# Performance work log

Measured on AMD Instinct MI355X. Metric: run time of the kernel, lower is better.

Reference implementation:

```python
import jax, jax.numpy as jnp
import numpy as np

B, S, H, L, NH, DH, FF = 64, 128, 768, 6, 12, 64, 3072
VOCAB, MAXPOS, INTENT, TAGS = 30522, 512, 22, 122
LN_EPS = 1e-12
INV_SQRT_DH = float(1.0 / np.sqrt(DH))


def _ln(x, s, b):
    m = x.mean(-1, keepdims=True)
    v = ((x - m) ** 2).mean(-1, keepdims=True)
    return (x - m) * jax.lax.rsqrt(v + LN_EPS) * s + b


def setup_inputs():
    key = jax.random.key(0)
    cnt = [0]
    def nk():
        cnt[0] += 1
        return jax.random.fold_in(key, cnt[0])
    def nrm(shape):
        return (0.02 * jax.random.normal(nk(), shape)).astype(jnp.float32)
    inp = {
        'input_ids': jax.random.randint(nk(), (B, S), 0, VOCAB),
        'attention_mask': jnp.ones((B, S), jnp.int32),
        'intent_target': jax.random.randint(nk(), (B,), 0, INTENT),
        'slots_target': jax.random.randint(nk(), (B, S), 0, TAGS),
        'slots_mask': jnp.ones((B, S), jnp.int32),
        'word_emb': nrm((VOCAB, H)), 'pos_emb': nrm((MAXPOS, H)),
        'emb_ln_s': jnp.ones((H,)), 'emb_ln_b': jnp.zeros((H,)),
        'Wq': nrm((L, H, H)), 'bq': jnp.zeros((L, H)),
        'Wk': nrm((L, H, H)), 'bk': jnp.zeros((L, H)),
        'Wv': nrm((L, H, H)), 'bv': jnp.zeros((L, H)),
        'Wo': nrm((L, H, H)), 'bo': jnp.zeros((L, H)),
        'sa_ln_s': jnp.ones((L, H)), 'sa_ln_b': jnp.zeros((L, H)),
        'W1f': nrm((L, H, FF)), 'b1f': jnp.zeros((L, FF)),
        'W2f': nrm((L, FF, H)), 'b2f': jnp.zeros((L, H)),
        'out_ln_s': jnp.ones((L, H)), 'out_ln_b': jnp.zeros((L, H)),
        'iW1': nrm((H, 64)), 'ib1': jnp.zeros((64,)),
        'iW2': nrm((64, INTENT)), 'ib2': jnp.zeros((INTENT,)),
        'sW1': nrm((H, 256)), 'sb1': jnp.zeros((256,)),
        'sW2': nrm((256, TAGS)), 'sb2': jnp.zeros((TAGS,)),
        'crf_start': nrm((TAGS,)), 'crf_end': nrm((TAGS,)), 'crf_trans': nrm((TAGS, TAGS)),
        'log_vars': jnp.zeros((2,)),
    }
    return inp


def _encoder(input_ids, attention_mask, word_emb, pos_emb, emb_ln_s, emb_ln_b,
             Wq, bq, Wk, bk, Wv, bv, Wo, bo, sa_ln_s, sa_ln_b,
             W1f, b1f, W2f, b2f, out_ln_s, out_ln_b):
    x = word_emb[input_ids] + pos_emb[jnp.arange(S)][None]
    x = _ln(x, emb_ln_s, emb_ln_b)
    neg = jnp.where(attention_mask[:, None, None, :] > 0, 0.0, -1e9).astype(x.dtype)
    for i in range(L):
        q = (x @ Wq[i] + bq[i]).reshape(B, S, NH, DH).transpose(0, 2, 1, 3)
        k = (x @ Wk[i] + bk[i]).reshape(B, S, NH, DH).transpose(0, 2, 1, 3)
        v = (x @ Wv[i] + bv[i]).reshape(B, S, NH, DH).transpose(0, 2, 1, 3)
        scores = jnp.einsum('bhqd,bhkd->bhqk', q, k) * INV_SQRT_DH + neg
        attn = jax.nn.softmax(scores, -1)
        ctx = jnp.einsum('bhqk,bhkd->bhqd', attn, v).transpose(0, 2, 1, 3).reshape(B, S, H)
        x = _ln(x + ctx @ Wo[i] + bo[i], sa_ln_s[i], sa_ln_b[i])
        h = jax.nn.gelu(x @ W1f[i] + b1f[i], approximate=False) @ W2f[i] + b2f[i]
        x = _ln(x + h, out_ln_s[i], out_ln_b[i])
    return x


def _crf_llh(emis, tags, mask, crf_start, crf_end, crf_trans):
    # pytorch-crf log-likelihood, reduction='sum'. emis [B,S,T], mask bool [B,S]
    fmask = mask.astype(emis.dtype)
    emit_sc = jnp.take_along_axis(emis, tags[..., None], -1)[..., 0]          # [B,S]
    trans_sc = crf_trans[tags[:, :-1], tags[:, 1:]]                            # [B,S-1]
    last_idx = mask.sum(1) - 1
    last_tag = tags[jnp.arange(B), last_idx]
    num = (crf_start[tags[:, 0]] + emit_sc[:, 0]
           + ((trans_sc + emit_sc[:, 1:]) * fmask[:, 1:]).sum(1)
           + crf_end[last_tag])
    def fstep(alpha, xs):
        emit_t, m_t = xs
        nxt = jax.nn.logsumexp(alpha[:, :, None] + crf_trans[None] + emit_t[:, None, :], axis=1)
        return jnp.where(m_t[:, None], nxt, alpha), None
    alpha0 = crf_start[None] + emis[:, 0]
    alpha, _ = jax.lax.scan(fstep, alpha0, (emis[:, 1:].transpose(1, 0, 2), mask[:, 1:].T))
    denom = jax.nn.logsumexp(alpha + crf_end[None], -1)
    return jnp.sum(num - denom)


def _viterbi(emis, mask, crf_start, crf_end, crf_trans):
    ident = jnp.arange(TAGS)[None, :]
    def vstep(alpha, xs):
        emit_t, m_t = xs
        score = alpha[:, :, None] + crf_trans[None] + emit_t[:, None, :]      # [B,T,T]
        bp = jnp.where(m_t[:, None], jnp.argmax(score, 1), ident)
        alpha = jnp.where(m_t[:, None], jnp.max(score, 1), alpha)
        return alpha, bp
    alpha0 = crf_start[None] + emis[:, 0]
    alpha, bps = jax.lax.scan(vstep, alpha0, (emis[:, 1:].transpose(1, 0, 2), mask[:, 1:].T))
    last = jnp.argmax(alpha + crf_end[None], -1)                               # [B]
    def bstep(tag, bp):
        prev = jnp.take_along_axis(bp, tag[:, None], 1)[:, 0]
        return prev, prev
    _, prevs = jax.lax.scan(bstep, last, bps, reverse=True)                    # [S-1,B]
    return jnp.concatenate([prevs, last[None]], 0).T                           # [B,S]


def reference(input_ids, attention_mask, intent_target, slots_target, slots_mask,
              word_emb, pos_emb, emb_ln_s, emb_ln_b,
              Wq, bq, Wk, bk, Wv, bv, Wo, bo, sa_ln_s, sa_ln_b,
              W1f, b1f, W2f, b2f, out_ln_s, out_ln_b,
              iW1, ib1, iW2, ib2, sW1, sb1, sW2, sb2,
              crf_start, crf_end, crf_trans, log_vars):
    x = _encoder(input_ids, attention_mask, word_emb, pos_emb, emb_ln_s, emb_ln_b,
                 Wq, bq, Wk, bk, Wv, bv, Wo, bo, sa_ln_s, sa_ln_b,
                 W1f, b1f, W2f, b2f, out_ln_s, out_ln_b)
    # intent head: linear1(relu(cls)) -> relu -> linear2 (dropout = eval identity)
    intent_logits = jax.nn.relu(jax.nn.relu(x[:, 0]) @ iW1 + ib1) @ iW2 + ib2
    intent_loss = (jax.nn.logsumexp(intent_logits, -1)
                   - jnp.take_along_axis(intent_logits, intent_target[:, None], 1)[:, 0])
    intent_pred = jnp.argmax(intent_logits, -1)
    # slots head
    slots_logits = jax.nn.relu(jax.nn.relu(x) @ sW1 + sb1) @ sW2 + sb2
    mask = slots_mask.astype(bool)
    slots_loss = -_crf_llh(slots_logits, slots_target, mask, crf_start, crf_end, crf_trans)
    p1 = jnp.exp(-log_vars[0])
    p2 = jnp.exp(-log_vars[1])
    joint_loss = jnp.sum(p1 * intent_loss + log_vars[0]) + (p2 * slots_loss + log_vars[1])
    slots_pred = _viterbi(slots_logits, mask, crf_start, crf_end, crf_trans)
    return joint_loss, slots_pred, intent_pred
```

## Files before the change

### kernel.cpp

```cpp
#include <hip/hip_runtime.h>
#include <math.h>
#include <stdint.h>

#define B_      64
#define S_      128
#define H_      768
#define L_      6
#define NH_     12
#define DH_     64
#define FF_     3072
#define INTENT_ 22
#define TAGS_   122
#define NT_     (B_*S_)
#define LN_EPS  1e-12f
#define INV_SQRT_DH 0.125f

#define GF_RELU_OUT 2
#define GF_GELU_OUT 4
#define GF_ADDRES   16
#define GF_ACCH     32

typedef _Float16 half8 __attribute__((ext_vector_type(8)));
typedef float    f32x4 __attribute__((ext_vector_type(4)));

__device__ __forceinline__ void gld16(const _Float16* g, _Float16* l) {
    __builtin_amdgcn_global_load_lds(
        (const __attribute__((address_space(1))) unsigned int*)(uintptr_t)g,
        (__attribute__((address_space(3))) unsigned int*)(unsigned int)(uintptr_t)l,
        16, 0, 0);
}

__device__ inline float wave_max(float v){
    #pragma unroll
    for (int d = 32; d; d >>= 1) v = fmaxf(v, __shfl_xor(v, d));
    return v;
}
__device__ inline float wave_sum(float v){
    #pragma unroll
    for (int d = 32; d; d >>= 1) v += __shfl_xor(v, d);
    return v;
}

__global__ __launch_bounds__(256) void embed_ln_kernel(
    const int* __restrict__ ids, const float* __restrict__ we,
    const float* __restrict__ pe, const float* __restrict__ gs,
    const float* __restrict__ gb, _Float16* __restrict__ Xh,
    _Float16* __restrict__ Xl)
{
    __shared__ float red[256];
    int bs = blockIdx.x;
    int sq = bs % S_;
    int id = ids[bs];
    int tid = threadIdx.x;
    const float* wrow = we + (size_t)id * H_;
    const float* prow = pe + (size_t)sq * H_;
    float z[3];
    #pragma unroll
    for (int r = 0; r < 3; r++) {
        int h = tid + 256*r;
        z[r] = wrow[h] + prow[h];
    }
    float sum = z[0]+z[1]+z[2];
    red[tid] = sum; __syncthreads();
    for (int off = 128; off > 0; off >>= 1) {
        if (tid < off) red[tid] += red[tid+off];
        __syncthreads();
    }
    float m = red[0] * (1.0f/H_); __syncthreads();
    float vs = 0.f;
    #pragma unroll
    for (int r = 0; r < 3; r++) { float d = z[r]-m; vs += d*d; }
    red[tid] = vs; __syncthreads();
    for (int off = 128; off > 0; off >>= 1) {
        if (tid < off) red[tid] += red[tid+off];
        __syncthreads();
    }
    float rstd = 1.0f / sqrtf(red[0]*(1.0f/H_) + LN_EPS);
    #pragma unroll
    for (int r = 0; r < 3; r++) {
        int h = tid + 256*r;
        float val = (z[r]-m)*rstd*gs[h] + gb[h];
        _Float16 hv = (_Float16)val;
        Xh[(size_t)bs*H_ + h] = hv;
        Xl[(size_t)bs*H_ + h] = (_Float16)(val - (float)hv);
    }
}

__global__ __launch_bounds__(384) void ln2_kernel(
    const _Float16* __restrict__ Sh, const _Float16* __restrict__ Sl,
    const float* __restrict__ gs, const float* __restrict__ gb,
    _Float16* __restrict__ Xh, _Float16* __restrict__ Xl,
    _Float16* __restrict__ Rh, _Float16* __restrict__ Rl)
{
    __shared__ float red[512];
    int bs = blockIdx.x, tid = threadIdx.x;
    size_t base = (size_t)bs*H_ + tid*2;
    union UU { _Float16 h[2]; unsigned u; };
    UU uh, ul;
    uh.u = *(const unsigned*)(Sh + base);
    ul.u = *(const unsigned*)(Sl + base);
    float z0 = (float)uh.h[0] + (float)ul.h[0];
    float z1 = (float)uh.h[1] + (float)ul.h[1];
    red[tid] = z0 + z1;
    if (tid < 128) red[384+tid] = 0.f;
    __syncthreads();
    for (int off = 256; off > 0; off >>= 1) {
        if (tid < off) red[tid] += red[tid+off];
        __syncthreads();
    }
    float m = red[0] * (1.0f/H_);
    __syncthreads();
    float d0 = z0-m, d1 = z1-m;
    red[tid] = d0*d0 + d1*d1;
    if (tid < 128) red[384+tid] = 0.f;
    __syncthreads();
    for (int off = 256; off > 0; off >>= 1) {
        if (tid < off) red[tid] += red[tid+off];
        __syncthreads();
    }
    float rstd = 1.0f / sqrtf(red[0]*(1.0f/H_) + LN_EPS);
    float2 gv = *(const float2*)(gs + tid*2);
    float2 bv = *(const float2*)(gb + tid*2);
    float v0 = d0*rstd*gv.x + bv.x;
    float v1 = d1*rstd*gv.y + bv.y;
    UU oh, ol;
    oh.h[0] = (_Float16)v0; ol.h[0] = (_Float16)(v0 - (float)oh.h[0]);
    oh.h[1] = (_Float16)v1; ol.h[1] = (_Float16)(v1 - (float)oh.h[1]);
    *(unsigned*)(Xh + base) = oh.u;
    *(unsigned*)(Xl + base) = ol.u;
    if (Rh) {
        float r0 = fmaxf(v0, 0.f), r1 = fmaxf(v1, 0.f);
        UU rh, rl;
        rh.h[0] = (_Float16)r0; rl.h[0] = (_Float16)(r0 - (float)rh.h[0]);
        rh.h[1] = (_Float16)r1; rl.h[1] = (_Float16)(r1 - (float)rh.h[1]);
        *(unsigned*)(Rh + base) = rh.u;
        *(unsigned*)(Rl + base) = rl.u;
    }
}

__global__ __launch_bounds__(256) void wconv_kernel(
    const float* __restrict__ W0, const float* __restrict__ W1,
    const float* __restrict__ W2, const float* __restrict__ W3,
    int K, int N, _Float16* __restrict__ OH, _Float16* __restrict__ OL, long zoff)
{
    __shared__ float t[64][65];
    int z = blockIdx.z;
    const float* W = (z==0) ? W0 : ((z==1) ? W1 : ((z==2) ? W2 : W3));
    OH += (long)z*zoff; OL += (long)z*zoff;
    int k0 = blockIdx.x*64, n0 = blockIdx.y*64;
    int tid = threadIdx.x;
    int lr = tid>>4, lc = (tid&15)*4;
    #pragma unroll
    for (int p = 0; p < 4; p++) {
        float4 v = *(const float4*)&W[(size_t)(k0+lr+16*p)*N + n0 + lc];
        t[lr+16*p][lc]   = v.x; t[lr+16*p][lc+1] = v.y;
        t[lr+16*p][lc+2] = v.z; t[lr+16*p][lc+3] = v.w;
    }
    __syncthreads();
    int n = tid>>2, kb = (tid&3)*16;
    union U { _Float16 h[8]; uint4 u; } h0, h1, l0, l1;
    #pragma unroll
    for (int e = 0; e < 8; e++) {
        float x = t[kb+e][n];
        _Float16 hv = (_Float16)x;
        h0.h[e] = hv; l0.h[e] = (_Float16)(x - (float)hv);
    }
    #pragma unroll
    for (int e = 0; e < 8; e++) {
        float x = t[kb+8+e][n];
        _Float16 hv = (_Float16)x;
        h1.h[e] = hv; l1.h[e] = (_Float16)(x - (float)hv);
    }
    size_t ob = (size_t)(n0+n)*K + k0 + kb;
    *(uint4*)&OH[ob]   = h0.u;
    *(uint4*)&OH[ob+8] = h1.u;
    *(uint4*)&OL[ob]   = l0.u;
    *(uint4*)&OL[ob+8] = l1.u;
}

__global__ __launch_bounds__(256) void gemm3_kernel(
    const _Float16* __restrict__ AhG, const _Float16* __restrict__ AlG, int lda,
    const _Float16* __restrict__ WtHb, const _Float16* __restrict__ WtLb,
    int ldw, long wz,
    float* __restrict__ C, _Float16* __restrict__ OHb, _Float16* __restrict__ OLb,
    int ldc, long oz,
    const _Float16* __restrict__ Rh, const _Float16* __restrict__ Rl, int ldr,
    const float* __restrict__ bias0, const float* __restrict__ bias1,
    const float* __restrict__ bias2,
    int K, int flags)
{
    __shared__ __align__(16) _Float16 Ah[128*32], Al[128*32];
    __shared__ __align__(16) _Float16 Bh[128*32], Bl[128*32];
    const int z = blockIdx.z;
    const _Float16* WtH = WtHb + (long)z*wz;
    const _Float16* WtL = WtLb + (long)z*wz;
    _Float16* oh = OHb ? OHb + (long)z*oz : (_Float16*)0;
    _Float16* ol = OLb ? OLb + (long)z*oz : (_Float16*)0;
    const float* bias = (z==0) ? bias0 : ((z==1) ? bias1 : bias2);
    const int tid = threadIdx.x, lane = tid&63, wid = tid>>6;
    const int wm = wid&1, wn = wid>>1;
    const int l15 = lane&15, quad = lane>>4;
    const int m0 = blockIdx.x*128, n0 = blockIdx.y*128;

    const _Float16* gsrc; _Float16* lbuf; int ld_s; int r0;
    if (wid == 0)      { gsrc = AhG; lbuf = Ah; ld_s = lda; r0 = m0; }
    else if (wid == 1) { gsrc = AlG; lbuf = Al; ld_s = lda; r0 = m0; }
    else if (wid == 2) { gsrc = WtH; lbuf = Bh; ld_s = ldw; r0 = n0; }
    else               { gsrc = WtL; lbuf = Bl; ld_s = ldw; r0 = n0; }
    const int kch = (lane&3) ^ ((lane>>3)&3);
    const _Float16* gbase = gsrc + (size_t)(r0 + (lane>>2))*ld_s + kch*8;

    const int slot = quad ^ ((l15>>1)&3);

    f32x4 acc[4][4];
    #pragma unroll
    for (int i = 0; i < 4; i++)
        #pragma unroll
        for (int j = 0; j < 4; j++)
            acc[i][j] = (f32x4){0.f,0.f,0.f,0.f};

    for (int k0 = 0; k0 < K; k0 += 32) {
        #pragma unroll
        for (int q = 0; q < 8; q++)
            gld16(gbase + (size_t)(q*16)*ld_s + k0, lbuf + q*512);
        __syncthreads();
        half8 afh[4], afl[4], bfh[4], bfl[4];
        #pragma unroll
        for (int i = 0; i < 4; i++) {
            int m = wm*64 + i*16 + l15;
            afh[i] = *(const half8*)&Ah[m*32 + slot*8];
            afl[i] = *(const half8*)&Al[m*32 + slot*8];
            int n = wn*64 + i*16 + l15;
            bfh[i] = *(const half8*)&Bh[n*32 + slot*8];
            bfl[i] = *(const half8*)&Bl[n*32 + slot*8];
        }
        #pragma unroll
        for (int i = 0; i < 4; i++)
            #pragma unroll
            for (int j = 0; j < 4; j++) {
                acc[i][j] = __builtin_amdgcn_mfma_f32_16x16x32_f16(afh[i], bfh[j], acc[i][j], 0,0,0);
                acc[i][j] = __builtin_amdgcn_mfma_f32_16x16x32_f16(afh[i], bfl[j], acc[i][j], 0,0,0);
                acc[i][j] = __builtin_amdgcn_mfma_f32_16x16x32_f16(afl[i], bfh[j], acc[i][j], 0,0,0);
            }
        __syncthreads();
    }
    #pragma unroll
    for (int i = 0; i < 4; i++)
        #pragma unroll
        for (int j = 0; j < 4; j++)
            #pragma unroll
            for (int r = 0; r < 4; r++) {
                int gm = m0 + wm*64 + i*16 + quad*4 + r;
                int gn = n0 + wn*64 + j*16 + l15;
                float v = acc[i][j][r];
                if (bias) v += bias[gn];
                size_t ox = (size_t)gm*ldc + gn;
                if (flags & GF_ADDRES) {
                    size_t rx = (size_t)gm*ldr + gn;
                    v += (float)Rh[rx] + (float)Rl[rx];
                }
                if (flags & GF_ACCH)
                    v += (float)oh[ox] + (float)ol[ox];
                if (flags & GF_RELU_OUT) v = fmaxf(v, 0.f);
                if (flags & GF_GELU_OUT) v = 0.5f*v*(1.0f + erff(v*0.70710678118654752f));
                if (oh) {
                    _Float16 hv = (_Float16)v;
                    oh[ox] = hv;
                    ol[ox] = (_Float16)(v - (float)hv);
                } else {
                    C[ox] = v;
                }
            }
}

#define BM 64
#define BN 64
#define BK 16
__global__ __launch_bounds__(256) void gemm_kernel(
    const float* __restrict__ A, int lda,
    const float* __restrict__ W, int ldb,
    float* __restrict__ C, int ldc,
    const float* __restrict__ bias,
    int M, int N, int K)
{
    __shared__ __align__(16) float As[BK][BM+4];
    __shared__ __align__(16) float Bs[BK][BN+4];
    int tid = threadIdx.x;
    int tx = tid & 15, ty = tid >> 4;
    int m0 = blockIdx.x * BM;
    int n0 = blockIdx.y * BN;
    float acc[4][4] = {};
    for (int k0 = 0; k0 < K; k0 += BK) {
        #pragma unroll
        for (int r = 0; r < 4; r++) {
            int li = tid + 256*r;
            int m  = li >> 4;
            int kk = li & 15;
            int gm = m0 + m, gk = k0 + kk;
            As[kk][m] = (gm < M && gk < K) ? A[(size_t)gm*lda + gk] : 0.f;
        }
        #pragma unroll
        for (int r = 0; r < 4; r++) {
            int li = tid + 256*r;
            int kk = li >> 6;
            int n  = li & 63;
            int gk = k0 + kk, gn = n0 + n;
            Bs[kk][n] = (gk < K && gn < N) ? W[(size_t)gk*ldb + gn] : 0.f;
        }
        __syncthreads();
        #pragma unroll
        for (int kk = 0; kk < BK; kk++) {
            float4 a  = *(const float4*)&As[kk][ty*4];
            float4 bb = *(const float4*)&Bs[kk][tx*4];
            float av[4] = {a.x, a.y, a.z, a.w};
            float bv[4] = {bb.x, bb.y, bb.z, bb.w};
            #pragma unroll
            for (int i = 0; i < 4; i++)
                #pragma unroll
                for (int j = 0; j < 4; j++)
                    acc[i][j] += av[i] * bv[j];
        }
        __syncthreads();
    }
    #pragma unroll
    for (int i = 0; i < 4; i++) {
        int gm = m0 + ty*4 + i;
        if (gm >= M) continue;
        #pragma unroll
        for (int j = 0; j < 4; j++) {
            int gn = n0 + tx*4 + j;
            if (gn >= N) continue;
            float v = acc[i][j];
            if (bias) v += bias[gn];
            C[(size_t)gm*ldc + gn] = v;
        }
    }
}

__device__ inline int scidx(int row, int col) {
    return row*128 + (((col>>2) ^ (row&7))<<2) + (col&3);
}
__global__ __launch_bounds__(256) void attn2_kernel(
    const _Float16* __restrict__ QhG, const _Float16* __restrict__ QlG,
    const _Float16* __restrict__ KhG, const _Float16* __restrict__ KlG,
    const _Float16* __restrict__ VhG, const _Float16* __restrict__ VlG,
    const int* __restrict__ amask,
    _Float16* __restrict__ Ch, _Float16* __restrict__ Cl)
{
    __shared__ __align__(16) char smem[65536];
    _Float16* Qh_s = (_Float16*)smem;
    _Float16* Ql_s = Qh_s + 64*72;
    _Float16* Kh_s = Ql_s + 64*72;
    _Float16* Kl_s = Kh_s + 128*72;
    float*    Sc   = (float*)smem;
    _Float16* Vth  = (_Float16*)(smem + 32768);
    _Float16* Vtl  = Vth + 64*128;

    int blk = blockIdx.x;
    int qh2 = blk & 1;
    int bh  = blk >> 1;
    int b = bh / NH_, hh = bh % NH_;
    const int tid = threadIdx.x, lane = tid&63, wid = tid>>6;
    const int l15 = lane&15, quad = lane>>4;
    const int qr = wid*16;
    size_t tokb = (size_t)b*S_*H_ + (size_t)hh*DH_;

    float nmask[8];
    #pragma unroll
    for (int j = 0; j < 8; j++)
        nmask[j] = (amask[b*S_ + j*16 + l15] > 0) ? 0.f : -1e9f;

    {
        int row = tid>>2, part = (tid&3)*16;
        size_t qg = tokb + (size_t)(qh2*64 + row)*H_ + part;
        *(uint4*)&Qh_s[row*72 + part] = *(const uint4*)(QhG + qg);
        *(uint4*)&Ql_s[row*72 + part] = *(const uint4*)(QlG + qg);
        #pragma unroll
        for (int p = 0; p < 2; p++) {
            int krow = row + p*64;
            size_t kg = tokb + (size_t)krow*H_ + part;
            *(uint4*)&Kh_s[krow*72 + part] = *(const uint4*)(KhG + kg);
            *(uint4*)&Kl_s[krow*72 + part] = *(const uint4*)(KlG + kg);
        }
    }
    __syncthreads();

    f32x4 acc1[8];
    #pragma unroll
    for (int j = 0; j < 8; j++) acc1[j] = (f32x4){0.f,0.f,0.f,0.f};
    half8 aqh[2], aql[2];
    #pragma unroll
    for (int kc = 0; kc < 2; kc++) {
        aqh[kc] = *(const half8*)&Qh_s[(qr + l15)*72 + kc*32 + quad*8];
        aql[kc] = *(const half8*)&Ql_s[(qr + l15)*72 + kc*32 + quad*8];
    }
    #pragma unroll
    for (int j = 0; j < 8; j++) {
        #pragma unroll
        for (int kc = 0; kc < 2; kc++) {
            half8 bkh = *(const half8*)&Kh_s[(j*16 + l15)*72 + kc*32 + quad*8];
            half8 bkl = *(const half8*)&Kl_s[(j*16 + l15)*72 + kc*32 + quad*8];
            acc1[j] = __builtin_amdgcn_mfma_f32_16x16x32_f16(aqh[kc], bkh, acc1[j], 0,0,0);
            acc1[j] = __builtin_amdgcn_mfma_f32_16x16x32_f16(aqh[kc], bkl, acc1[j], 0,0,0);
            acc1[j] = __builtin_amdgcn_mfma_f32_16x16x32_f16(aql[kc], bkh, acc1[j], 0,0,0);
        }
    }
    __syncthreads();

    #pragma unroll
    for (int j = 0; j < 8; j++)
        #pragma unroll
        for (int r = 0; r < 4; r++) {
            int row = qr + quad*4 + r;
            int col = j*16 + l15;
            Sc[scidx(row, col)] = acc1[j][r]*INV_SQRT_DH + nmask[j];
        }
    {
        int key = tid>>1, dh = (tid&1)*32;
        union V32 { _Float16 h[32]; uint4 u[4]; } bufh, bufl;
        #pragma unroll
        for (int e = 0; e < 4; e++) {
            bufh.u[e] = *(const uint4*)(VhG + tokb + (size_t)key*H_ + dh + e*8);
            bufl.u[e] = *(const uint4*)(VlG + tokb + (size_t)key*H_ + dh + e*8);
        }
        int kg = key>>3, kr = key&7;
        #pragma unroll
        for (int e = 0; e < 32; e++) {
            int d = dh + e;
            int pos = kg ^ (d & 7);
            Vth[d*128 + pos*8 + kr] = bufh.h[e];
            Vtl[d*128 + pos*8 + kr] = bufl.h[e];
        }
    }
    __syncthreads();

    {
        int row = tid>>2, part = (tid&3)*32;
        float mx = -INFINITY;
        #pragma unroll 8
        for (int e = 0; e < 32; e++)
            mx = fmaxf(mx, Sc[scidx(row, part+e)]);
        mx = fmaxf(mx, __shfl_xor(mx, 1));
        mx = fmaxf(mx, __shfl_xor(mx, 2));
        float s = 0.f;
        #pragma unroll 8
        for (int e = 0; e < 32; e++) {
            int idx = scidx(row, part+e);
            float ev = expf(Sc[idx] - mx);
            Sc[idx] = ev; s += ev;
        }
        s += __shfl_xor(s, 1);
        s += __shfl_xor(s, 2);
        float inv = 1.0f / s;
        #pragma unroll 8
        for (int e = 0; e < 32; e++)
            Sc[scidx(row, part+e)] *= inv;
    }
    __syncthreads();

    f32x4 acc2[4];
    #pragma unroll
    for (int jd = 0; jd < 4; jd++) acc2[jd] = (f32x4){0.f,0.f,0.f,0.f};
    #pragma unroll
    for (int kc = 0; kc < 4; kc++) {
        int q = qr + l15;
        int g16 = kc*8 + quad*2;
        float4 p0 = *(const float4*)&Sc[q*128 + ((g16   ^ (q&7))<<2)];
        float4 p1 = *(const float4*)&Sc[q*128 + (((g16+1) ^ (q&7))<<2)];
        float pv[8] = {p0.x,p0.y,p0.z,p0.w, p1.x,p1.y,p1.z,p1.w};
        union U { _Float16 h[8]; half8 v; } ph, pl;
        #pragma unroll
        for (int e = 0; e < 8; e++) {
            _Float16 hv = (_Float16)pv[e];
            ph.h[e] = hv; pl.h[e] = (_Float16)(pv[e] - (float)hv);
        }
        #pragma unroll
        for (int jd = 0; jd < 4; jd++) {
            int n = jd*16 + l15;
            int pos = (kc*4 + quad) ^ (n & 7);
            half8 vh = *(const half8*)&Vth[n*128 + pos*8];
            half8 vl = *(const half8*)&Vtl[n*128 + pos*8];
            acc2[jd] = __builtin_amdgcn_mfma_f32_16x16x32_f16(ph.v, vh, acc2[jd], 0,0,0);
            acc2[jd] = __builtin_amdgcn_mfma_f32_16x16x32_f16(ph.v, vl, acc2[jd], 0,0,0);
            acc2[jd] = __builtin_amdgcn_mfma_f32_16x16x32_f16(pl.v, vh, acc2[jd], 0,0,0);
        }
    }
    #pragma unroll
    for (int jd = 0; jd < 4; jd++)
        #pragma unroll
        for (int r = 0; r < 4; r++) {
            int row = qr + quad*4 + r;
            int token = b*S_ + qh2*64 + row;
            int d = jd*16 + l15;
            float v = acc2[jd][r];
            _Float16 hv = (_Float16)v;
            Ch[(size_t)token*H_ + hh*DH_ + d] = hv;
            Cl[(size_t)token*H_ + hh*DH_ + d] = (_Float16)(v - (float)hv);
        }
}

__global__ __launch_bounds__(64) void intent_kernel(
    const _Float16* __restrict__ Xh, const _Float16* __restrict__ Xl,
    const float* __restrict__ iW1,
    const float* __restrict__ ib1, const float* __restrict__ iW2,
    const float* __restrict__ ib2, const int* __restrict__ tgt,
    float* __restrict__ iloss, float* __restrict__ outf)
{
    int b = blockIdx.x; int j = threadIdx.x;
    __shared__ float h1[64];
    __shared__ float lg[32];
    const _Float16* x0h = Xh + (size_t)b*S_*H_;
    const _Float16* x0l = Xl + (size_t)b*S_*H_;
    float acc = ib1[j];
    for (int h = 0; h < H_; h++) {
        float x = (float)x0h[h] + (float)x0l[h];
        acc += fmaxf(x, 0.f) * iW1[(size_t)h*64 + j];
    }
    h1[j] = fmaxf(acc, 0.f);
    __syncthreads();
    if (j < INTENT_) {
        float l = ib2[j];
        for (int k = 0; k < 64; k++) l += h1[k]*iW2[k*INTENT_ + j];
        lg[j] = l;
    }
    __syncthreads();
    if (j == 0) {
        float mx = -INFINITY; int bi = 0;
        for (int c = 0; c < INTENT_; c++) if (lg[c] > mx) { mx = lg[c]; bi = c; }
        float sm = 0.f;
        for (int c = 0; c < INTENT_; c++) sm += expf(lg[c]-mx);
        float lse = mx + logf(sm);
        iloss[b] = lse - lg[tgt[b]];
        outf[1 + (size_t)NT_ + b] = (float)bi;
    }
}

#define VST 130
__global__ __launch_bounds__(512) void crf_vit_kernel(
    const float* __restrict__ E_, const int* __restrict__ tags,
    const int* __restrict__ mask, const float* __restrict__ start,
    const float* __restrict__ endv, const float* __restrict__ trans,
    float* __restrict__ crfv, unsigned char* __restrict__ BPg,
    float* __restrict__ outf)
{
    __shared__ __align__(16) float tT[TAGS_*VST];
    __shared__ __align__(16) float eal[2][128];
    __shared__ float mxw[2][8];
    __shared__ float mxbuf[16];
    __shared__ int lastt;
    int b = blockIdx.x;
    int mode = blockIdx.y;
    int tid = threadIdx.x, lane = tid&63, wid = tid>>6;
    int j = tid>>2, p = tid&3;
    int cnt = (p < 2) ? 31 : 30;
    bool vj = (j < TAGS_);
    const float* E = E_ + (size_t)b*S_*TAGS_;

    if (vj) {
        for (int e = 0; e < cnt; e++) {
            int i = 4*e + p;
            float tv = trans[i*TAGS_ + j];
            tT[j*VST + i] = mode ? tv : expf(tv);
        }
    }
    float aj = vj ? (start[j] + E[j]) : -3e38f;

    if (mode == 0) {
        {
            float wm = wave_max(aj);
            if (lane == 0) mxw[0][wid] = wm;
        }
        __syncthreads();
        float gm = mxw[0][0];
        #pragma unroll
        for (int w = 1; w < 8; w++) gm = fmaxf(gm, mxw[0][w]);
        float xc = gm;
        if (p == 0) eal[0][j] = vj ? expf(aj - xc) : 0.f;
        __syncthreads();
        int cur = 0;
        float eC = vj ? E[(size_t)TAGS_ + j] : 0.f;
        int   mC = mask[b*S_ + 1];
        for (int t = 1; t < S_; t++) {
            float e = eC; int m_t = mC;
            if (t + 1 < S_) {
                eC = vj ? E[(size_t)(t+1)*TAGS_ + j] : 0.f;
                mC = mask[b*S_ + t + 1];
            }
            float s = 0.f;
            if (vj) {
                const float* tr = &tT[j*VST];
                const float* eb = &eal[cur][0];
                float sa = 0.f, sb = 0.f;
                for (int e2 = 0; e2 + 1 < cnt; e2 += 2) {
                    int i0 = 4*e2 + p, i1 = 4*e2 + 4 + p;
                    sa += eb[i0] * tr[i0];
                    sb += eb[i1] * tr[i1];
                }
                if (cnt & 1) { int il = 4*(cnt-1) + p; sa += eb[il] * tr[il]; }
                s = sa + sb;
            }
            s += __shfl_xor(s, 1);
            s += __shfl_xor(s, 2);
            if (m_t && vj) aj = xc + logf(s) + e;
            int nxt = cur ^ 1;
            float xn = gm;
            if (p == 0) eal[nxt][j] = vj ? expf(aj - xn) : 0.f;
            float wm2 = wave_max(aj);
            if (lane == 0) mxw[nxt][wid] = wm2;
            __syncthreads();
            float nm = mxw[nxt][0];
            #pragma unroll
            for (int w = 1; w < 8; w++) nm = fmaxf(nm, mxw[nxt][w]);
            gm = nm;
            xc = xn;
            cur = nxt;
        }
        if (p == 0) eal[0][j] = aj;
        float term = 0.f, mkf = 0.f;
        if (tid < S_) {
            int mk = mask[b*S_ + tid]; mkf = (float)mk;
            if (tid >= 1 && mk) {
                int tg = tags[b*S_ + tid], tgp = tags[b*S_ + tid - 1];
                term = trans[tgp*TAGS_ + tg] + E[(size_t)tid*TAGS_ + tg];
            }
        }
        if (wid < 2) {
            float ts = wave_sum(term);
            float ms = wave_sum(mkf);
            if (lane == 0) { mxbuf[2+wid] = ts; mxbuf[4+wid] = ms; }
        }
        __syncthreads();
        if (wid == 0) {
            const float* alp = &eal[0][0];
            float v1 = (lane < TAGS_) ? alp[lane] + endv[lane] : -3e38f;
            float v2 = (lane+64 < TAGS_) ? alp[lane+64] + endv[lane+64] : -3e38f;
            float m = wave_max(fmaxf(v1, v2));
            float sd = ((lane < TAGS_) ? expf(v1 - m) : 0.f)
                     + ((lane+64 < TAGS_) ? expf(v2 - m) : 0.f);
            sd = wave_sum(sd);
            if (lane == 0) {
                float denom = m + logf(sd);
                float numsum = mxbuf[2] + mxbuf[3];
                int msum = (int)(mxbuf[4] + mxbuf[5]);
                int tag0 = tags[b*S_];
                int last_tag = tags[b*S_ + (msum - 1)];
                float num = start[tag0] + E[tag0] + numsum + endv[last_tag];
                crfv[b] = num - denom;
            }
        }
    } else {
        if (p == 0) eal[0][j] = aj;
        __syncthreads();
        int cur = 0;
        size_t bpb = (size_t)b*(S_-1)*TAGS_;
        float eC = vj ? E[(size_t)TAGS_ + j] : 0.f;
        int   mC = mask[b*S_ + 1];
        for (int t = 1; t < S_; t++) {
            float ee = eC; int m_t = mC;
            if (t + 1 < S_) {
                eC = vj ? E[(size_t)(t+1)*TAGS_ + j] : 0.f;
                mC = mask[b*S_ + t + 1];
            }
            float best = -3e38f; int bi = 0;
            if (vj) {
                const float* tr = &tT[j*VST];
                const float* ab = &eal[cur][0];
                for (int e = 0; e < cnt; e++) {
                    int i = 4*e + p;
                    float v = ab[i] + tr[i];
                    if (v > best) { best = v; bi = i; }
                }
            }
            {
                float ov = __shfl_xor(best, 1); int oi = __shfl_xor(bi, 1);
                if (ov > best || (ov == best && oi < bi)) { best = ov; bi = oi; }
                ov = __shfl_xor(best, 2); oi = __shfl_xor(bi, 2);
                if (ov > best || (ov == best && oi < bi)) { best = ov; bi = oi; }
            }
            float nv; int nb;
            if (m_t) { nv = best + ee; nb = bi; }
            else     { nv = aj; nb = j; }
            int nxt = cur ^ 1;
            if (vj) {
                aj = nv;
                if (p == 0) {
                    eal[nxt][j] = aj;
                    BPg[bpb + (size_t)(t-1)*TAGS_ + j] = (unsigned char)nb;
                }
            }
            __syncthreads();
            cur = nxt;
        }
        if (p == 0) eal[0][j] = aj;
        __syncthreads();
        if (wid == 0) {
            const float* alp = &eal[0][0];
            float v; int idx;
            float v1 = (lane < TAGS_) ? alp[lane] + endv[lane] : -3e38f;
            float v2 = (lane+64 < TAGS_) ? alp[lane+64] + endv[lane+64] : -3e38f;
            if (v2 > v1) { v = v2; idx = lane+64; } else { v = v1; idx = lane; }
            #pragma unroll
            for (int d = 32; d; d >>= 1) {
                float ov = __shfl_xor(v, d); int oi = __shfl_xor(idx, d);
                if (ov > v || (ov == v && oi < idx)) { v = ov; idx = oi; }
            }
            if (lane == 0) lastt = idx;
        }
        __syncthreads();
        unsigned char* bpl = (unsigned char*)tT;
        for (int o = tid; o < (S_-1)*TAGS_; o += 512)
            bpl[o] = BPg[bpb + o];
        __syncthreads();
        if (tid == 0) {
            int tag = lastt;
            outf[1 + (size_t)b*S_ + (S_-1)] = (float)tag;
            for (int t = S_-1; t >= 1; t--) {
                tag = bpl[(t-1)*TAGS_ + tag];
                outf[1 + (size_t)b*S_ + (t-1)] = (float)tag;
            }
        }
    }
}

__global__ void combine_kernel(const float* __restrict__ iloss,
                               const float* __restrict__ crfv,
                               const float* __restrict__ lv,
                               float* __restrict__ outf)
{
    if (threadIdx.x == 0 && blockIdx.x == 0) {
        float si = 0.f, sc = 0.f;
        for (int b = 0; b < B_; b++) { si += iloss[b]; sc += crfv[b]; }
        float p1 = expf(-lv[0]), p2 = expf(-lv[1]);
        float slots_loss = -sc;
        outf[0] = p1*si + (float)B_*lv[0] + p2*slots_loss + lv[1];
    }
}

extern "C" void kernel_launch(void* const* d_in, const int* in_sizes, int n_in,
                              void* d_out, int out_size, void* d_ws, size_t ws_size,
                              hipStream_t stream) {
    const int*   ids   = (const int*)  d_in[0];
    const int*   amask = (const int*)  d_in[1];
    const int*   itgt  = (const int*)  d_in[2];
    const int*   stgt  = (const int*)  d_in[3];
    const int*   smask = (const int*)  d_in[4];
    const float* we    = (const float*)d_in[5];
    const float* pe    = (const float*)d_in[6];
    const float* embs  = (const float*)d_in[7];
    const float* embb  = (const float*)d_in[8];
    const float* Wq    = (const float*)d_in[9];
    const float* bq    = (const float*)d_in[10];
    const float* Wk    = (const float*)d_in[11];
    const float* bk    = (const float*)d_in[12];
    const float* Wv    = (const float*)d_in[13];
    const float* bv    = (const float*)d_in[14];
    const float* Wo    = (const float*)d_in[15];
    const float* bo    = (const float*)d_in[16];
    const float* sas   = (const float*)d_in[17];
    const float* sab   = (const float*)d_in[18];
    const float* W1f   = (const float*)d_in[19];
    const float* b1f   = (const float*)d_in[20];
    const float* W2f   = (const float*)d_in[21];
    const float* b2f   = (const float*)d_in[22];
    const float* ols   = (const float*)d_in[23];
    const float* olb   = (const float*)d_in[24];
    const float* iW1   = (const float*)d_in[25];
    const float* ib1   = (const float*)d_in[26];
    const float* iW2   = (const float*)d_in[27];
    const float* ib2   = (const float*)d_in[28];
    const float* sW1   = (const float*)d_in[29];
    const float* sb1   = (const float*)d_in[30];
    const float* sW2   = (const float*)d_in[31];
    const float* sb2   = (const float*)d_in[32];
    const float* crfs  = (const float*)d_in[33];
    const float* crfe  = (const float*)d_in[34];
    const float* crft  = (const float*)d_in[35];
    const float* lv    = (const float*)d_in[36];

    float* outf = (float*)d_out;
    float* wsf  = (float*)d_ws;
    const long NTHh = (long)NT_ * H_;
    const long NBf  = NTHh;
    const long HH   = (long)H_ * H_;

    _Float16* Xh = (_Float16*)wsf;
    _Float16* Xl = Xh + NTHh;
    float*    Pf = wsf + NBf;
    _Float16* Ph = (_Float16*)Pf;
    _Float16 *Qh = Ph, *Ql = Ph + NTHh, *Kh = Ph + 2*NTHh, *Kl = Ph + 3*NTHh,
             *Vh = Ph + 4*NTHh, *Vl = Ph + 5*NTHh;
    _Float16 *Sh = Ph, *Sl = Ph + NTHh;
    _Float16* Fh = (_Float16*)(wsf + 2*NBf);
    _Float16* Fl = (_Float16*)(wsf + 3*NBf);
    _Float16* Ch = (_Float16*)(wsf + 4*NBf);
    _Float16* Cl = Ch + NTHh;
    const long wa0 = 5*NBf;
    _Float16* WAh = (_Float16*)(wsf + wa0);
    _Float16* WAl = WAh + 4*HH;
    const long wb1 = wa0 + 2359296;
    _Float16* WB1h = (_Float16*)(wsf + wb1);
    _Float16* WB1l = WB1h + 2359296;
    const long wb2 = wb1 + 2359296;
    _Float16* WB2h = (_Float16*)(wsf + wb2);
    _Float16* WB2l = WB2h + 2359296;
    float* iloss = wsf + wb2 + 2359296;
    float* crfv  = iloss + 64;
    float* H1 = Pf;
    float* logits = Pf + 2097152;
    unsigned char* BPg = (unsigned char*)(Pf + 2097152 + 999424);

    auto g3 = [&](int gy, int gz,
                  const _Float16* A_h, const _Float16* A_l, int lda,
                  const _Float16* WtH, const _Float16* WtL, int ldw, long wz,
                  float* C, _Float16* OH, _Float16* OL, int ldc, long oz,
                  const _Float16* Rh, const _Float16* Rl,
                  const float* b0, const float* b1_, const float* b2_,
                  int K, int flags) {
        hipLaunchKernelGGL(gemm3_kernel, dim3(NT_/128, gy, gz), dim3(256), 0, stream,
                           A_h, A_l, lda, WtH, WtL, ldw, wz,
                           C, OH, OL, ldc, oz, Rh, Rl, H_, b0, b1_, b2_, K, flags);
    };

    hipLaunchKernelGGL(embed_ln_kernel, dim3(NT_), dim3(256), 0, stream,
                       ids, we, pe, embs, embb, Xh, Xl);

    for (int i = 0; i < L_; i++) {
        const long WO = (long)i*HH;
        hipLaunchKernelGGL(wconv_kernel, dim3(12,12,4), dim3(256), 0, stream,
                           Wq+WO, Wk+WO, Wv+WO, Wo+WO, H_, H_, WAh, WAl, HH);
        g3(6, 3, Xh, Xl, H_, WAh, WAl, H_, HH,
           nullptr, Ph, Ph+NTHh, H_, 2*NTHh, nullptr, nullptr,
           bq+i*H_, bk+i*H_, bv+i*H_, H_, 0);
        hipLaunchKernelGGL(attn2_kernel, dim3(B_*NH_*2), dim3(256), 0, stream,
                           Qh, Ql, Kh, Kl, Vh, Vl, amask, Ch, Cl);
        g3(6, 1, Ch, Cl, H_, WAh+3*HH, WAl+3*HH, H_, 0,
           nullptr, Sh, Sl, H_, 0, Xh, Xl,
           bo+i*H_, nullptr, nullptr, H_, GF_ADDRES);
        hipLaunchKernelGGL(ln2_kernel, dim3(NT_), dim3(384), 0, stream,
                           Sh, Sl, sas+i*H_, sab+i*H_, Xh, Xl,
                           (_Float16*)nullptr, (_Float16*)nullptr);
        hipLaunchKernelGGL(wconv_kernel, dim3(12,48,1), dim3(256), 0, stream,
                           W1f+(long)i*H_*FF_, nullptr, nullptr, nullptr,
                           H_, FF_, WB1h, WB1l, 0);
        hipLaunchKernelGGL(wconv_kernel, dim3(48,12,1), dim3(256), 0, stream,
                           W2f+(long)i*FF_*H_, nullptr, nullptr, nullptr,
                           FF_, H_, WB2h, WB2l, 0);
        for (int c = 0; c < 2; c++) {
            const int CW = FF_/2;
            g3(12, 1, Xh, Xl, H_,
               WB1h+(long)c*CW*H_, WB1l+(long)c*CW*H_, H_, 0,
               nullptr, Fh, Fl, CW, 0, nullptr, nullptr,
               b1f+(long)i*FF_+c*CW, nullptr, nullptr, H_, GF_GELU_OUT);
            g3(6, 1, Fh, Fl, CW,
               WB2h+(long)c*CW, WB2l+(long)c*CW, FF_, 0,
               nullptr, Sh, Sl, H_, 0, Xh, Xl,
               (c==0) ? (b2f+i*H_) : nullptr, nullptr, nullptr,
               CW, (c==0) ? GF_ADDRES : GF_ACCH);
        }
        hipLaunchKernelGGL(ln2_kernel, dim3(NT_), dim3(384), 0, stream,
                           Sh, Sl, ols+i*H_, olb+i*H_, Xh, Xl,
                           (i==L_-1) ? Ch : (_Float16*)nullptr,
                           (i==L_-1) ? Cl : (_Float16*)nullptr);
    }

    hipLaunchKernelGGL(intent_kernel, dim3(B_), dim3(64), 0, stream,
                       Xh, Xl, iW1, ib1, iW2, ib2, itgt, iloss, outf);

    hipLaunchKernelGGL(wconv_kernel, dim3(12,4,1), dim3(256), 0, stream,
                       sW1, nullptr, nullptr, nullptr, H_, 256,
                       WAh, WAh + (long)256*H_, 0);
    g3(2, 1, Ch, Cl, H_, WAh, WAh + (long)256*H_, H_, 0,
       H1, nullptr, nullptr, 256, 0, nullptr, nullptr,
       sb1, nullptr, nullptr, H_, GF_RELU_OUT);
    hipLaunchKernelGGL(gemm_kernel, dim3(NT_/BM, 2), dim3(256), 0, stream,
                       H1, 256, sW2, TAGS_, logits, TAGS_, sb2, NT_, TAGS_, 256);

    hipLaunchKernelGGL(crf_vit_kernel, dim3(B_, 2), dim3(512), 0, stream,
                       logits, stgt, smask, crfs, crfe, crft, crfv, BPg, outf);

    hipLaunchKernelGGL(combine_kernel, dim3(1), dim3(64), 0, stream,
                       iloss, crfv, lv, outf);
}
```

Measured before the change: 4.808 ms.

## Use wave-shuffle LayerNorm reductions and contiguous float4 CRF/Viterbi inner loops

The embedding and residual LayerNorm kernels now reduce with wave shuffles plus one small shared-memory combine, replacing the shared-memory tree with many barriers. The CRF forward and Viterbi kernels re-lay out the transposed transition table so each of the four lanes per tag covers a contiguous 32-element chunk, zero-padded, and reads it with float4 loads. Tags beyond the valid range now write neutral values to eal so the padded slots are harmless. This is meant to cut barrier count and shared-memory instruction count in latency-bound sequential loops. The risk is subtle tie-breaking or padding errors in the argmax.

```diff
diff --git a/kernel.cpp b/kernel.cpp
--- a/kernel.cpp
+++ b/kernel.cpp
@@ -47,11 +47,12 @@
     const float* __restrict__ gb, _Float16* __restrict__ Xh,
     _Float16* __restrict__ Xl)
 {
-    __shared__ float red[256];
+    __shared__ float red[16];
     int bs = blockIdx.x;
     int sq = bs % S_;
     int id = ids[bs];
     int tid = threadIdx.x;
+    int lane = tid & 63, wid = tid >> 6;
     const float* wrow = we + (size_t)id * H_;
     const float* prow = pe + (size_t)sq * H_;
     float z[3];
@@ -60,22 +61,17 @@
         int h = tid + 256*r;
         z[r] = wrow[h] + prow[h];
     }
-    float sum = z[0]+z[1]+z[2];
-    red[tid] = sum; __syncthreads();
-    for (int off = 128; off > 0; off >>= 1) {
-        if (tid < off) red[tid] += red[tid+off];
-        __syncthreads();
-    }
-    float m = red[0] * (1.0f/H_); __syncthreads();
+    float s1 = wave_sum(z[0]+z[1]+z[2]);
+    if (lane == 0) red[wid] = s1;
+    __syncthreads();
+    float m = (red[0]+red[1]+red[2]+red[3]) * (1.0f/H_);
     float vs = 0.f;
     #pragma unroll
     for (int r = 0; r < 3; r++) { float d = z[r]-m; vs += d*d; }
-    red[tid] = vs; __syncthreads();
-    for (int off = 128; off > 0; off >>= 1) {
-        if (tid < off) red[tid] += red[tid+off];
-        __syncthreads();
-    }
-    float rstd = 1.0f / sqrtf(red[0]*(1.0f/H_) + LN_EPS);
+    float s2 = wave_sum(vs);
+    if (lane == 0) red[8+wid] = s2;
+    __syncthreads();
+    float rstd = 1.0f / sqrtf((red[8]+red[9]+red[10]+red[11])*(1.0f/H_) + LN_EPS);
     #pragma unroll
     for (int r = 0; r < 3; r++) {
         int h = tid + 256*r;
@@ -92,8 +88,9 @@
     _Float16* __restrict__ Xh, _Float16* __restrict__ Xl,
     _Float16* __restrict__ Rh, _Float16* __restrict__ Rl)
 {
-    __shared__ float red[512];
+    __shared__ float red[16];
     int bs = blockIdx.x, tid = threadIdx.x;
+    int lane = tid & 63, wid = tid >> 6;
     size_t base = (size_t)bs*H_ + tid*2;
     union UU { _Float16 h[2]; unsigned u; };
     UU uh, ul;
@@ -101,24 +98,16 @@
     ul.u = *(const unsigned*)(Sl + base);
     float z0 = (float)uh.h[0] + (float)ul.h[0];
     float z1 = (float)uh.h[1] + (float)ul.h[1];
-    red[tid] = z0 + z1;
-    if (tid < 128) red[384+tid] = 0.f;
-    __syncthreads();
-    for (int off = 256; off > 0; off >>= 1) {
-        if (tid < off) red[tid] += red[tid+off];
-        __syncthreads();
-    }
-    float m = red[0] * (1.0f/H_);
-    __syncthreads();
+    float s1 = wave_sum(z0 + z1);
+    if (lane == 0) red[wid] = s1;
+    __syncthreads();
+    float m = (red[0]+red[1]+red[2]+red[3]+red[4]+red[5]) * (1.0f/H_);
     float d0 = z0-m, d1 = z1-m;
-    red[tid] = d0*d0 + d1*d1;
-    if (tid < 128) red[384+tid] = 0.f;
-    __syncthreads();
-    for (int off = 256; off > 0; off >>= 1) {
-        if (tid < off) red[tid] += red[tid+off];
-        __syncthreads();
-    }
-    float rstd = 1.0f / sqrtf(red[0]*(1.0f/H_) + LN_EPS);
+    float s2 = wave_sum(d0*d0 + d1*d1);
+    if (lane == 0) red[8+wid] = s2;
+    __syncthreads();
+    float var = (red[8]+red[9]+red[10]+red[11]+red[12]+red[13]) * (1.0f/H_);
+    float rstd = 1.0f / sqrtf(var + LN_EPS);
     float2 gv = *(const float2*)(gs + tid*2);
     float2 bv = *(const float2*)(gb + tid*2);
     float v0 = d0*rstd*gv.x + bv.x;
@@ -535,7 +524,7 @@
     }
 }
 
-#define VST 130
+#define VST 124
 __global__ __launch_bounds__(512) void crf_vit_kernel(
     const float* __restrict__ E_, const int* __restrict__ tags,
     const int* __restrict__ mask, const float* __restrict__ start,
@@ -552,18 +541,20 @@
     int mode = blockIdx.y;
     int tid = threadIdx.x, lane = tid&63, wid = tid>>6;
     int j = tid>>2, p = tid&3;
-    int cnt = (p < 2) ? 31 : 30;
     bool vj = (j < TAGS_);
     const float* E = E_ + (size_t)b*S_*TAGS_;
 
-    if (vj) {
-        for (int e = 0; e < cnt; e++) {
-            int i = 4*e + p;
-            float tv = trans[i*TAGS_ + j];
-            tT[j*VST + i] = mode ? tv : expf(tv);
-        }
+    for (int o = tid; o < TAGS_*VST; o += 512) {
+        int jj = o / VST, i = o - jj*VST;
+        float v;
+        if (i < TAGS_) {
+            float tv = trans[i*TAGS_ + jj];
+            v = mode ? tv : expf(tv);
+        } else v = 0.f;
+        tT[o] = v;
     }
     float aj = vj ? (start[j] + E[j]) : -3e38f;
+    const int ibase = 32*p;
 
     if (mode == 0) {
         {
@@ -588,16 +579,17 @@
             }
             float s = 0.f;
             if (vj) {
-                const float* tr = &tT[j*VST];
-                const float* eb = &eal[cur][0];
-                float sa = 0.f, sb = 0.f;
-                for (int e2 = 0; e2 + 1 < cnt; e2 += 2) {
-                    int i0 = 4*e2 + p, i1 = 4*e2 + 4 + p;
-                    sa += eb[i0] * tr[i0];
-                    sb += eb[i1] * tr[i1];
+                const float4* tr = (const float4*)&tT[j*VST + ibase];
+                const float4* eb = (const float4*)&eal[cur][ibase];
+                float s0 = 0.f, s1 = 0.f, s2 = 0.f, s3 = 0.f;
+                #pragma unroll
+                for (int q = 0; q < 8; q++) {
+                    float4 av = eb[q];
+                    float4 tv = tr[q];
+                    s0 += av.x*tv.x; s1 += av.y*tv.y;
+                    s2 += av.z*tv.z; s3 += av.w*tv.w;
                 }
-                if (cnt & 1) { int il = 4*(cnt-1) + p; sa += eb[il] * tr[il]; }
-                s = sa + sb;
+                s = (s0 + s1) + (s2 + s3);
             }
             s += __shfl_xor(s, 1);
             s += __shfl_xor(s, 2);
@@ -663,13 +655,24 @@
             }
             float best = -3e38f; int bi = 0;
             if (vj) {
-                const float* tr = &tT[j*VST];
-                const float* ab = &eal[cur][0];
-                for (int e = 0; e < cnt; e++) {
-                    int i = 4*e + p;
-                    float v = ab[i] + tr[i];
-                    if (v > best) { best = v; bi = i; }
+                const float4* tr = (const float4*)&tT[j*VST + ibase];
+                const float4* ab = (const float4*)&eal[cur][ibase];
+                float b0 = -3e38f, b1 = -3e38f, b2 = -3e38f, b3 = -3e38f;
+                int i0 = ibase, i1 = ibase+1, i2 = ibase+2, i3 = ibase+3;
+                #pragma unroll
+                for (int q = 0; q < 8; q++) {
+                    float4 av = ab[q];
+                    float4 tv = tr[q];
+                    float c;
+                    c = av.x + tv.x; if (c > b0) { b0 = c; i0 = ibase+4*q; }
+                    c = av.y + tv.y; if (c > b1) { b1 = c; i1 = ibase+4*q+1; }
+                    c = av.z + tv.z; if (c > b2) { b2 = c; i2 = ibase+4*q+2; }
+                    c = av.w + tv.w; if (c > b3) { b3 = c; i3 = ibase+4*q+3; }
                 }
+                best = b0; bi = i0;
+                if (b1 > best || (b1 == best && i1 < bi)) { best = b1; bi = i1; }
+                if (b2 > best || (b2 == best && i2 < bi)) { best = b2; bi = i2; }
+                if (b3 > best || (b3 == best && i3 < bi)) { best = b3; bi = i3; }
             }
             {
                 float ov = __shfl_xor(best, 1); int oi = __shfl_xor(bi, 1);
@@ -681,13 +684,10 @@
             if (m_t) { nv = best + ee; nb = bi; }
             else     { nv = aj; nb = j; }
             int nxt = cur ^ 1;
-            if (vj) {
-                aj = nv;
-                if (p == 0) {
-                    eal[nxt][j] = aj;
-                    BPg[bpb + (size_t)(t-1)*TAGS_ + j] = (unsigned char)nb;
-                }
-            }
+            if (vj) aj = nv;
+            if (p == 0) eal[nxt][j] = aj;
+            if (vj && p == 0)
+                BPg[bpb + (size_t)(t-1)*TAGS_ + j] = (unsigned char)nb;
             __syncthreads();
             cur = nxt;
         }
```

New measurement: 4.701 ms. -2.2%, faster.
